# Performance work log

Hardware: AMD Instinct MI355X
Metric: run time of the kernel (lower is better)

## Reference

```python
import jax, jax.numpy as jnp
import numpy as np

BLOCK_SIZE = 2048
HEAD_SIZE = 64
N_EMBD = 768


def setup_inputs() -> dict:
    key = jax.random.key(0)
    k1, k2, k3 = jax.random.split(key, 3)
    x = jax.random.normal(k1, (8, 2048, N_EMBD), dtype=jnp.float32)
    Wq = jax.random.normal(k2, (N_EMBD, HEAD_SIZE), dtype=jnp.float32) * (N_EMBD ** -0.5)
    rel_table = jax.random.normal(k3, (2 * BLOCK_SIZE - 1, 1), dtype=jnp.float32)
    return {"x": x, "Wq": Wq, "rel_table": rel_table}


def reference(x, Wq, rel_table):
    B, T, C = x.shape
    # NOTE: original module uses self.query for q, k AND v (faithful reproduction)
    q = x @ Wq  # [B, T, H]
    k = q
    v = q
    max_rel = BLOCK_SIZE - 1
    pos = jnp.arange(T)
    rel = pos[None, :] - pos[:, None]            # [T, T]
    rel_idx = jnp.clip(rel, -max_rel, max_rel) + max_rel
    bias = rel_table[rel_idx, 0][None, :, :]     # [1, T, T]
    scores = jnp.einsum('bth,bsh->bts', q, k) * (HEAD_SIZE ** -0.5)
    scores = scores + bias
    causal = pos[None, :] <= pos[:, None]        # [T, T] lower-triangular
    scores = jnp.where(causal[None, :, :], scores, -jnp.inf)
    attn = jax.nn.softmax(scores, axis=-1)       # dropout p=0.0 -> identity
    out = jnp.einsum('bts,bsh->bth', attn, v)    # [B, T, H]
    return out
```

## Files before the change

### kernel.cpp

```cpp
#include <hip/hip_runtime.h>
#include <hip/hip_fp16.h>

typedef _Float16 half8 __attribute__((ext_vector_type(8)));
typedef _Float16 half4 __attribute__((ext_vector_type(4)));
typedef float floatx4 __attribute__((ext_vector_type(4)));

#define T_SEQ 2048
#define NB    8

#define GLOBAL_AS __attribute__((address_space(1)))
#define LDS_AS    __attribute__((address_space(3)))

__global__ __launch_bounds__(256) void prep_kernel(
    const float* __restrict__ Wq, const float* __restrict__ rel,
    _Float16* __restrict__ WqT, float* __restrict__ biasS)
{
  const int bid = blockIdx.x, tid = threadIdx.x;
  if (bid < 64) {
    for (int k = tid; k < 768; k += 256)
      WqT[bid * 768 + k] = (_Float16)Wq[k * 64 + bid];
  } else {
    for (int i = tid; i < 4095; i += 256)
      biasS[i] = rel[i] * 1.44269504f;
  }
}

__global__ __launch_bounds__(256, 2) void qproj_kernel(
    const float* __restrict__ x, const _Float16* __restrict__ WqT,
    const float* __restrict__ rel,
    _Float16* __restrict__ q16, _Float16* __restrict__ q16T,
    float* __restrict__ Ct)
{
  __shared__ __align__(16) float xbuf[16 * 772];
  __shared__ float part[2 * 16 * 66];
  __shared__ float sumsq[16];
  _Float16* qs = (_Float16*)xbuf;

  const int tid  = threadIdx.x;
  const int w    = tid >> 6, lane = tid & 63;
  const int n    = lane & 15, quad = lane >> 4;
  const int k0   = w * 192;

  const _Float16* wp = WqT + (size_t)n * 768 + k0 + quad * 8;
  half8 Breg[6][4];
  #pragma unroll
  for (int i = 0; i < 6; ++i)
    #pragma unroll
    for (int t = 0; t < 4; ++t)
      Breg[i][t] = *(const half8*)(wp + 32 * i + t * 16 * 768);

  const float b0v = rel[2047] * 1.44269504f;
  float* partw = part + (w & 1) * 1056;

  #pragma unroll 1
  for (int it = 0; it < 2; ++it) {
    const int r0 = (blockIdx.x + it * 512) * 16;

    __syncthreads();

    #pragma unroll
    for (int r = 0; r < 4; ++r) {
      #pragma unroll
      for (int c = 0; c < 3; ++c) {
        const float* gp = x + (size_t)(r0 + 4 * w + r) * 768 + c * 256 + lane * 4;
        float* lp = xbuf + (4 * w + r) * 772 + c * 256 + lane * 4;
        __builtin_amdgcn_global_load_lds((const GLOBAL_AS void*)gp,
                                         (LDS_AS void*)lp, 16, 0, 0);
      }
    }
    __builtin_amdgcn_s_waitcnt(0x0f70);
    __syncthreads();

    floatx4 acc[4];
    #pragma unroll
    for (int s = 0; s < 4; ++s) acc[s] = (floatx4){0.f, 0.f, 0.f, 0.f};

    #pragma unroll
    for (int i = 0; i < 6; ++i) {
      const float* ap = xbuf + n * 772 + k0 + 32 * i + quad * 8;
      float4 x0 = *(const float4*)ap;
      float4 x1 = *(const float4*)(ap + 4);
      half8 a;
      a[0] = (_Float16)x0.x; a[1] = (_Float16)x0.y;
      a[2] = (_Float16)x0.z; a[3] = (_Float16)x0.w;
      a[4] = (_Float16)x1.x; a[5] = (_Float16)x1.y;
      a[6] = (_Float16)x1.z; a[7] = (_Float16)x1.w;
      acc[0] = __builtin_amdgcn_mfma_f32_16x16x32_f16(a, Breg[i][0], acc[0], 0, 0, 0);
      acc[1] = __builtin_amdgcn_mfma_f32_16x16x32_f16(a, Breg[i][1], acc[1], 0, 0, 0);
      acc[2] = __builtin_amdgcn_mfma_f32_16x16x32_f16(a, Breg[i][2], acc[2], 0, 0, 0);
      acc[3] = __builtin_amdgcn_mfma_f32_16x16x32_f16(a, Breg[i][3], acc[3], 0, 0, 0);
    }

    if (w < 2) {
      #pragma unroll
      for (int sub = 0; sub < 4; ++sub)
        #pragma unroll
        for (int r = 0; r < 4; ++r)
          partw[(4 * quad + r) * 66 + sub * 16 + n] = acc[sub][r];
    }
    __syncthreads();
    if (w >= 2) {
      #pragma unroll
      for (int sub = 0; sub < 4; ++sub)
        #pragma unroll
        for (int r = 0; r < 4; ++r)
          partw[(4 * quad + r) * 66 + sub * 16 + n] += acc[sub][r];
    }
    __syncthreads();

    #pragma unroll
    for (int k = 0; k < 4; ++k) {
      int e = tid + k * 256;
      int row = e >> 6, h = e & 63;
      float s = part[row * 66 + h] + part[1056 + row * 66 + h];
      q16[(size_t)(r0 + row) * 64 + h] = (_Float16)s;
      qs[row * 66 + h] = (_Float16)s;
      float ss = s * s;
      #pragma unroll
      for (int off = 1; off < 64; off <<= 1) ss += __shfl_xor(ss, off);
      if (lane == 0) sumsq[row] = ss;
    }
    __syncthreads();

    if (tid < 16)
      Ct[r0 + tid] = sumsq[tid] * 0.18033688f + b0v + 8.0f;

    {
      const int h = tid >> 2, rq = (tid & 3) * 4;
      half4 hv;
      hv[0] = qs[(rq + 0) * 66 + h]; hv[1] = qs[(rq + 1) * 66 + h];
      hv[2] = qs[(rq + 2) * 66 + h]; hv[3] = qs[(rq + 3) * 66 + h];
      const int bb = r0 >> 11, tt = r0 & 2047;
      *(half4*)(q16T + (size_t)(bb * 64 + h) * T_SEQ + tt + rq) = hv;
    }
  }
}

__global__ __launch_bounds__(256, 2) void attn_kernel(
    const _Float16* __restrict__ q16, const _Float16* __restrict__ q16T,
    const float* __restrict__ biasS, const float* __restrict__ Ct,
    float* __restrict__ out)
{
  __shared__ __align__(16) _Float16 Pbuf[4 * 16 * 72];
  __shared__ float Obuf[4 * 16 * 65];
  __shared__ float Lbuf[4 * 16];
  __shared__ float biasL[2080];

  const int bi = blockIdx.x;
  const int b  = bi & 7;
  const int p  = bi >> 3;

  const int tid  = threadIdx.x;
  const int w    = tid >> 6;
  const int lane = tid & 63;
  const int n    = lane & 15, quad = lane >> 4;

  _Float16* Pw = Pbuf + w * 1152;
  const float ksc = 0.125f * 1.44269504f;
  const _Float16* vbase = q16T + (size_t)(b * 64 + n) * T_SEQ + quad * 8;
  const half8 ones = {(_Float16)1, (_Float16)1, (_Float16)1, (_Float16)1,
                      (_Float16)1, (_Float16)1, (_Float16)1, (_Float16)1};

  #define LOAD_KV(S0, K, V)                                                   \
    {                                                                         \
      _Pragma("unroll")                                                       \
      for (int sub = 0; sub < 4; ++sub) {                                     \
        const _Float16* kp =                                                  \
            q16 + (size_t)(b * T_SEQ + (S0) + sub * 16 + n) * 64 + quad * 8;  \
        K[2 * sub]     = *(const half8*)kp;                                   \
        K[2 * sub + 1] = *(const half8*)(kp + 32);                            \
      }                                                                       \
      _Pragma("unroll")                                                       \
      for (int sh = 0; sh < 4; ++sh) {                                        \
        V[sh]     = *(const half8*)(vbase + (size_t)(sh * 16) * T_SEQ + (S0));\
        V[4 + sh] = *(const half8*)(vbase + (size_t)(sh * 16) * T_SEQ + (S0) + 32); \
      }                                                                       \
    }

  #pragma unroll 1
  for (int ht = 0; ht < 2; ++ht) {
    const int qi = ht ? (127 - p) : p;
    const int t0 = qi * 16;
    const int kfull = t0 >> 6;

    {
      const int lo = 2032 - t0, cnt = t0 + 31;
      for (int i = tid; i < cnt; i += 256) biasL[i] = biasS[lo + i];
    }

    half8 aq0, aq1;
    {
      const _Float16* qrow = q16 + (size_t)(b * T_SEQ + t0 + n) * 64 + quad * 8;
      aq0 = *(const half8*)qrow;
      aq1 = *(const half8*)(qrow + 32);
    }
    float ctv[4];
    #pragma unroll
    for (int r = 0; r < 4; ++r)
      ctv[r] = Ct[b * T_SEQ + t0 + 4 * quad + r];

    floatx4 O[4];
    #pragma unroll
    for (int s = 0; s < 4; ++s) O[s] = (floatx4){0.f, 0.f, 0.f, 0.f};
    floatx4 den = (floatx4){0.f, 0.f, 0.f, 0.f};

    __syncthreads();

    half8 cK[8], cV[8], nK[8], nV[8];
    int kt = w;
    if (kt <= kfull) LOAD_KV(kt * 64, cK, cV);

    for (; kt <= kfull; kt += 4) {
      const int ktn = kt + 4;
      if (ktn <= kfull) LOAD_KV(ktn * 64, nK, nV);

      const int  s0 = kt * 64;
      const bool dg = (kt == kfull);
      const int  j  = (t0 - s0) >> 4;

      #pragma unroll
      for (int sub = 0; sub < 4; ++sub) {
        if (dg && sub > j) {
          #pragma unroll
          for (int r = 0; r < 4; ++r)
            Pw[(4 * quad + r) * 72 + sub * 16 + n] = (_Float16)0.f;
          continue;
        }
        floatx4 sc = (floatx4){0.f, 0.f, 0.f, 0.f};
        sc = __builtin_amdgcn_mfma_f32_16x16x32_f16(aq0, cK[2 * sub], sc, 0, 0, 0);
        sc = __builtin_amdgcn_mfma_f32_16x16x32_f16(aq1, cK[2 * sub + 1], sc, 0, 0, 0);
        const int smin = s0 + sub * 16;
        #pragma unroll
        for (int r = 0; r < 4; ++r) {
          float bv = biasL[15 + smin + n - 4 * quad - r];
          float pv = exp2f(fmaf(sc[r], ksc, bv) - ctv[r]);
          if (dg && sub == j && n > 4 * quad + r) pv = 0.f;
          Pw[(4 * quad + r) * 72 + sub * 16 + n] = (_Float16)pv;
        }
      }

      #pragma unroll
      for (int ch = 0; ch < 2; ++ch) {
        half8 pf = *(const half8*)(Pw + n * 72 + ch * 32 + quad * 8);
        den = __builtin_amdgcn_mfma_f32_16x16x32_f16(pf, ones, den, 0, 0, 0);
        #pragma unroll
        for (int sh = 0; sh < 4; ++sh)
          O[sh] = __builtin_amdgcn_mfma_f32_16x16x32_f16(pf, cV[ch * 4 + sh],
                                                         O[sh], 0, 0, 0);
      }

      #pragma unroll
      for (int i = 0; i < 8; ++i) { cK[i] = nK[i]; cV[i] = nV[i]; }
    }

    #pragma unroll
    for (int sub = 0; sub < 4; ++sub)
      #pragma unroll
      for (int r = 0; r < 4; ++r)
        Obuf[w * 1040 + (4 * quad + r) * 65 + sub * 16 + n] = O[sub][r];
    if (n == 0) {
      #pragma unroll
      for (int r = 0; r < 4; ++r)
        Lbuf[w * 16 + 4 * quad + r] = den[r];
    }
    __syncthreads();

    #pragma unroll
    for (int k = 0; k < 4; ++k) {
      const int e = tid + k * 256;
      const int row = e >> 6, h = e & 63;
      float num = Obuf[row * 65 + h]        + Obuf[1040 + row * 65 + h] +
                  Obuf[2080 + row * 65 + h] + Obuf[3120 + row * 65 + h];
      float d   = Lbuf[row] + Lbuf[16 + row] + Lbuf[32 + row] + Lbuf[48 + row];
      out[(size_t)(b * T_SEQ + t0 + row) * 64 + h] = num / d;
    }
  }
  #undef LOAD_KV
}

extern "C" void kernel_launch(void* const* d_in, const int* in_sizes, int n_in,
                              void* d_out, int out_size, void* d_ws, size_t ws_size,
                              hipStream_t stream) {
  const float* x   = (const float*)d_in[0];
  const float* Wq  = (const float*)d_in[1];
  const float* rel = (const float*)d_in[2];
  float* out = (float*)d_out;

  _Float16* q16   = (_Float16*)d_ws;
  _Float16* q16T  = q16  + (size_t)NB * T_SEQ * 64;
  _Float16* WqT   = q16T + (size_t)NB * T_SEQ * 64;
  float*    biasS = (float*)(WqT + 64 * 768);
  float*    Ct    = biasS + 4096;

  prep_kernel <<<65,  256, 0, stream>>>(Wq, rel, WqT, biasS);
  qproj_kernel<<<512, 256, 0, stream>>>(x, WqT, rel, q16, q16T, Ct);
  attn_kernel <<<512, 256, 0, stream>>>(q16, q16T, biasS, Ct, out);
}
```

Before: 134.9 us.

## Split persistent loops into one tile per block and pre-swizzle Wq fragments

The qproj and attention kernels no longer loop over two tiles per block; grids double to 1024 blocks and each block handles a single tile. Attention blocks pair light and heavy query tiles through index remapping instead of an inner loop. Wq is pre-packed in MFMA fragment order so qproj loads B fragments directly per chunk instead of holding them in registers, and x is converted to fp16 into LDS with plain loads rather than async LDS loads. The bias prescaling moves into the attention kernel, removing one prep buffer. This trades per-block setup reuse for more blocks, higher occupancy and better load balance.

```diff
diff --git a/kernel.cpp b/kernel.cpp
--- a/kernel.cpp
+++ b/kernel.cpp
@@ -8,137 +8,109 @@
 #define T_SEQ 2048
 #define NB    8
 
-#define GLOBAL_AS __attribute__((address_space(1)))
-#define LDS_AS    __attribute__((address_space(3)))
-
-__global__ __launch_bounds__(256) void prep_kernel(
-    const float* __restrict__ Wq, const float* __restrict__ rel,
-    _Float16* __restrict__ WqT, float* __restrict__ biasS)
+__global__ __launch_bounds__(64) void prep_kernel(
+    const float* __restrict__ Wq, _Float16* __restrict__ WqTs)
 {
-  const int bid = blockIdx.x, tid = threadIdx.x;
-  if (bid < 64) {
-    for (int k = tid; k < 768; k += 256)
-      WqT[bid * 768 + k] = (_Float16)Wq[k * 64 + bid];
-  } else {
-    for (int i = tid; i < 4095; i += 256)
-      biasS[i] = rel[i] * 1.44269504f;
-  }
-}
-
-__global__ __launch_bounds__(256, 2) void qproj_kernel(
-    const float* __restrict__ x, const _Float16* __restrict__ WqT,
+  const int b = blockIdx.x;
+  const int cg = b >> 2, t = b & 3;
+  const int l = threadIdx.x, n = l & 15, q = l >> 4;
+  const int h = 16 * t + n;
+  half8 v;
+  #pragma unroll
+  for (int j = 0; j < 8; ++j)
+    v[j] = (_Float16)Wq[(32 * cg + 8 * q + j) * 64 + h];
+  *(half8*)(WqTs + (size_t)b * 512 + l * 8) = v;
+}
+
+__global__ __launch_bounds__(256, 4) void qproj_kernel(
+    const float* __restrict__ x, const _Float16* __restrict__ WqTs,
     const float* __restrict__ rel,
     _Float16* __restrict__ q16, _Float16* __restrict__ q16T,
     float* __restrict__ Ct)
 {
-  __shared__ __align__(16) float xbuf[16 * 772];
-  __shared__ float part[2 * 16 * 66];
-  __shared__ float sumsq[16];
-  _Float16* qs = (_Float16*)xbuf;
+  __shared__ __align__(16) char smem[24704];
+  _Float16* xs   = (_Float16*)smem;
+  float*    cbuf = (float*)smem;
+  _Float16* qs   = (_Float16*)(smem + 16640);
+  float*    sq   = (float*)(smem + 16640 + 2112);
 
   const int tid  = threadIdx.x;
   const int w    = tid >> 6, lane = tid & 63;
   const int n    = lane & 15, quad = lane >> 4;
-  const int k0   = w * 192;
-
-  const _Float16* wp = WqT + (size_t)n * 768 + k0 + quad * 8;
-  half8 Breg[6][4];
-  #pragma unroll
-  for (int i = 0; i < 6; ++i)
-    #pragma unroll
-    for (int t = 0; t < 4; ++t)
-      Breg[i][t] = *(const half8*)(wp + 32 * i + t * 16 * 768);
+  const int r0   = blockIdx.x * 16;
+
+  #pragma unroll
+  for (int i = 0; i < 12; ++i) {
+    const int e   = tid + 256 * i;
+    const int row = e / 192, c4 = e - row * 192;
+    float4 v = *(const float4*)(x + (size_t)(r0 + row) * 768 + 4 * c4);
+    half4 hv;
+    hv[0] = (_Float16)v.x; hv[1] = (_Float16)v.y;
+    hv[2] = (_Float16)v.z; hv[3] = (_Float16)v.w;
+    *(half4*)(xs + row * 770 + 4 * c4) = hv;
+  }
+  __syncthreads();
+
+  floatx4 acc[4];
+  #pragma unroll
+  for (int s = 0; s < 4; ++s) acc[s] = (floatx4){0.f, 0.f, 0.f, 0.f};
+
+  const int k0 = w * 192;
+  #pragma unroll
+  for (int c = 0; c < 6; ++c) {
+    const int cg = w * 6 + c;
+    const _Float16* bp = WqTs + (size_t)cg * 2048 + lane * 8;
+    half8 b0 = *(const half8*)(bp);
+    half8 b1 = *(const half8*)(bp + 512);
+    half8 b2 = *(const half8*)(bp + 1024);
+    half8 b3 = *(const half8*)(bp + 1536);
+    half8 a  = *(const half8*)(xs + n * 770 + k0 + 32 * c + 8 * quad);
+    acc[0] = __builtin_amdgcn_mfma_f32_16x16x32_f16(a, b0, acc[0], 0, 0, 0);
+    acc[1] = __builtin_amdgcn_mfma_f32_16x16x32_f16(a, b1, acc[1], 0, 0, 0);
+    acc[2] = __builtin_amdgcn_mfma_f32_16x16x32_f16(a, b2, acc[2], 0, 0, 0);
+    acc[3] = __builtin_amdgcn_mfma_f32_16x16x32_f16(a, b3, acc[3], 0, 0, 0);
+  }
+  __syncthreads();
+
+  #pragma unroll
+  for (int sub = 0; sub < 4; ++sub)
+    #pragma unroll
+    for (int r = 0; r < 4; ++r)
+      cbuf[w * 1040 + (4 * quad + r) * 65 + sub * 16 + n] = acc[sub][r];
+  __syncthreads();
 
   const float b0v = rel[2047] * 1.44269504f;
-  float* partw = part + (w & 1) * 1056;
-
-  #pragma unroll 1
-  for (int it = 0; it < 2; ++it) {
-    const int r0 = (blockIdx.x + it * 512) * 16;
-
-    __syncthreads();
-
-    #pragma unroll
-    for (int r = 0; r < 4; ++r) {
-      #pragma unroll
-      for (int c = 0; c < 3; ++c) {
-        const float* gp = x + (size_t)(r0 + 4 * w + r) * 768 + c * 256 + lane * 4;
-        float* lp = xbuf + (4 * w + r) * 772 + c * 256 + lane * 4;
-        __builtin_amdgcn_global_load_lds((const GLOBAL_AS void*)gp,
-                                         (LDS_AS void*)lp, 16, 0, 0);
-      }
-    }
-    __builtin_amdgcn_s_waitcnt(0x0f70);
-    __syncthreads();
-
-    floatx4 acc[4];
-    #pragma unroll
-    for (int s = 0; s < 4; ++s) acc[s] = (floatx4){0.f, 0.f, 0.f, 0.f};
-
-    #pragma unroll
-    for (int i = 0; i < 6; ++i) {
-      const float* ap = xbuf + n * 772 + k0 + 32 * i + quad * 8;
-      float4 x0 = *(const float4*)ap;
-      float4 x1 = *(const float4*)(ap + 4);
-      half8 a;
-      a[0] = (_Float16)x0.x; a[1] = (_Float16)x0.y;
-      a[2] = (_Float16)x0.z; a[3] = (_Float16)x0.w;
-      a[4] = (_Float16)x1.x; a[5] = (_Float16)x1.y;
-      a[6] = (_Float16)x1.z; a[7] = (_Float16)x1.w;
-      acc[0] = __builtin_amdgcn_mfma_f32_16x16x32_f16(a, Breg[i][0], acc[0], 0, 0, 0);
-      acc[1] = __builtin_amdgcn_mfma_f32_16x16x32_f16(a, Breg[i][1], acc[1], 0, 0, 0);
-      acc[2] = __builtin_amdgcn_mfma_f32_16x16x32_f16(a, Breg[i][2], acc[2], 0, 0, 0);
-      acc[3] = __builtin_amdgcn_mfma_f32_16x16x32_f16(a, Breg[i][3], acc[3], 0, 0, 0);
-    }
-
-    if (w < 2) {
-      #pragma unroll
-      for (int sub = 0; sub < 4; ++sub)
-        #pragma unroll
-        for (int r = 0; r < 4; ++r)
-          partw[(4 * quad + r) * 66 + sub * 16 + n] = acc[sub][r];
-    }
-    __syncthreads();
-    if (w >= 2) {
-      #pragma unroll
-      for (int sub = 0; sub < 4; ++sub)
-        #pragma unroll
-        for (int r = 0; r < 4; ++r)
-          partw[(4 * quad + r) * 66 + sub * 16 + n] += acc[sub][r];
-    }
-    __syncthreads();
-
-    #pragma unroll
-    for (int k = 0; k < 4; ++k) {
-      int e = tid + k * 256;
-      int row = e >> 6, h = e & 63;
-      float s = part[row * 66 + h] + part[1056 + row * 66 + h];
-      q16[(size_t)(r0 + row) * 64 + h] = (_Float16)s;
-      qs[row * 66 + h] = (_Float16)s;
-      float ss = s * s;
-      #pragma unroll
-      for (int off = 1; off < 64; off <<= 1) ss += __shfl_xor(ss, off);
-      if (lane == 0) sumsq[row] = ss;
-    }
-    __syncthreads();
-
-    if (tid < 16)
-      Ct[r0 + tid] = sumsq[tid] * 0.18033688f + b0v + 8.0f;
-
-    {
-      const int h = tid >> 2, rq = (tid & 3) * 4;
-      half4 hv;
-      hv[0] = qs[(rq + 0) * 66 + h]; hv[1] = qs[(rq + 1) * 66 + h];
-      hv[2] = qs[(rq + 2) * 66 + h]; hv[3] = qs[(rq + 3) * 66 + h];
-      const int bb = r0 >> 11, tt = r0 & 2047;
-      *(half4*)(q16T + (size_t)(bb * 64 + h) * T_SEQ + tt + rq) = hv;
-    }
+  #pragma unroll
+  for (int k = 0; k < 4; ++k) {
+    const int e = tid + 256 * k;
+    const int row = e >> 6, h = e & 63;
+    float s = cbuf[row * 65 + h]        + cbuf[1040 + row * 65 + h] +
+              cbuf[2080 + row * 65 + h] + cbuf[3120 + row * 65 + h];
+    q16[(size_t)(r0 + row) * 64 + h] = (_Float16)s;
+    qs[row * 66 + h] = (_Float16)s;
+    float ss = s * s;
+    #pragma unroll
+    for (int off = 1; off < 64; off <<= 1) ss += __shfl_xor(ss, off);
+    if (lane == 0) sq[row] = ss;
+  }
+  __syncthreads();
+
+  if (tid < 16)
+    Ct[r0 + tid] = sq[tid] * 0.18033688f + b0v + 8.0f;
+
+  {
+    const int h = tid >> 2, rq = (tid & 3) * 4;
+    half4 hv;
+    hv[0] = qs[(rq + 0) * 66 + h]; hv[1] = qs[(rq + 1) * 66 + h];
+    hv[2] = qs[(rq + 2) * 66 + h]; hv[3] = qs[(rq + 3) * 66 + h];
+    const int bb = r0 >> 11, tt = r0 & 2047;
+    *(half4*)(q16T + (size_t)(bb * 64 + h) * T_SEQ + tt + rq) = hv;
   }
 }
 
 __global__ __launch_bounds__(256, 2) void attn_kernel(
     const _Float16* __restrict__ q16, const _Float16* __restrict__ q16T,
-    const float* __restrict__ biasS, const float* __restrict__ Ct,
+    const float* __restrict__ rel, const float* __restrict__ Ct,
     float* __restrict__ out)
 {
   __shared__ __align__(16) _Float16 Pbuf[4 * 16 * 72];
@@ -148,18 +120,44 @@
 
   const int bi = blockIdx.x;
   const int b  = bi & 7;
-  const int p  = bi >> 3;
+  const int u  = bi >> 3;
+  const int qi = (u < 64) ? u : 191 - u;
+  const int t0 = qi * 16;
+  const int kfull = t0 >> 6;
 
   const int tid  = threadIdx.x;
   const int w    = tid >> 6;
   const int lane = tid & 63;
   const int n    = lane & 15, quad = lane >> 4;
 
+  {
+    const int lo = 2032 - t0, cnt = t0 + 31;
+    for (int i = tid; i < cnt; i += 256) biasL[i] = rel[lo + i] * 1.44269504f;
+  }
+
+  half8 aq0, aq1;
+  {
+    const _Float16* qrow = q16 + (size_t)(b * T_SEQ + t0 + n) * 64 + quad * 8;
+    aq0 = *(const half8*)qrow;
+    aq1 = *(const half8*)(qrow + 32);
+  }
+  float ctv[4];
+  #pragma unroll
+  for (int r = 0; r < 4; ++r)
+    ctv[r] = Ct[b * T_SEQ + t0 + 4 * quad + r];
+
+  floatx4 O[4];
+  #pragma unroll
+  for (int s = 0; s < 4; ++s) O[s] = (floatx4){0.f, 0.f, 0.f, 0.f};
+  floatx4 den = (floatx4){0.f, 0.f, 0.f, 0.f};
+  const half8 ones = {(_Float16)1, (_Float16)1, (_Float16)1, (_Float16)1,
+                      (_Float16)1, (_Float16)1, (_Float16)1, (_Float16)1};
+
   _Float16* Pw = Pbuf + w * 1152;
   const float ksc = 0.125f * 1.44269504f;
   const _Float16* vbase = q16T + (size_t)(b * 64 + n) * T_SEQ + quad * 8;
-  const half8 ones = {(_Float16)1, (_Float16)1, (_Float16)1, (_Float16)1,
-                      (_Float16)1, (_Float16)1, (_Float16)1, (_Float16)1};
+
+  __syncthreads();
 
   #define LOAD_KV(S0, K, V)                                                   \
     {                                                                         \
@@ -177,105 +175,75 @@
       }                                                                       \
     }
 
-  #pragma unroll 1
-  for (int ht = 0; ht < 2; ++ht) {
-    const int qi = ht ? (127 - p) : p;
-    const int t0 = qi * 16;
-    const int kfull = t0 >> 6;
-
-    {
-      const int lo = 2032 - t0, cnt = t0 + 31;
-      for (int i = tid; i < cnt; i += 256) biasL[i] = biasS[lo + i];
+  half8 cK[8], cV[8], nK[8], nV[8];
+  int kt = w;
+  if (kt <= kfull) LOAD_KV(kt * 64, cK, cV);
+
+  for (; kt <= kfull; kt += 4) {
+    const int ktn = kt + 4;
+    if (ktn <= kfull) LOAD_KV(ktn * 64, nK, nV);
+
+    const int  s0 = kt * 64;
+    const bool dg = (kt == kfull);
+    const int  j  = (t0 - s0) >> 4;
+
+    #pragma unroll
+    for (int sub = 0; sub < 4; ++sub) {
+      if (dg && sub > j) {
+        #pragma unroll
+        for (int r = 0; r < 4; ++r)
+          Pw[(4 * quad + r) * 72 + sub * 16 + n] = (_Float16)0.f;
+        continue;
+      }
+      floatx4 sc = (floatx4){0.f, 0.f, 0.f, 0.f};
+      sc = __builtin_amdgcn_mfma_f32_16x16x32_f16(aq0, cK[2 * sub], sc, 0, 0, 0);
+      sc = __builtin_amdgcn_mfma_f32_16x16x32_f16(aq1, cK[2 * sub + 1], sc, 0, 0, 0);
+      const int smin = s0 + sub * 16;
+      #pragma unroll
+      for (int r = 0; r < 4; ++r) {
+        float bv = biasL[15 + smin + n - 4 * quad - r];
+        float pv = exp2f(fmaf(sc[r], ksc, bv) - ctv[r]);
+        if (dg && sub == j && n > 4 * quad + r) pv = 0.f;
+        Pw[(4 * quad + r) * 72 + sub * 16 + n] = (_Float16)pv;
+      }
     }
 
-    half8 aq0, aq1;
-    {
-      const _Float16* qrow = q16 + (size_t)(b * T_SEQ + t0 + n) * 64 + quad * 8;
-      aq0 = *(const half8*)qrow;
-      aq1 = *(const half8*)(qrow + 32);
+    #pragma unroll
+    for (int ch = 0; ch < 2; ++ch) {
+      half8 pf = *(const half8*)(Pw + n * 72 + ch * 32 + quad * 8);
+      den = __builtin_amdgcn_mfma_f32_16x16x32_f16(pf, ones, den, 0, 0, 0);
+      #pragma unroll
+      for (int sh = 0; sh < 4; ++sh)
+        O[sh] = __builtin_amdgcn_mfma_f32_16x16x32_f16(pf, cV[ch * 4 + sh],
+                                                       O[sh], 0, 0, 0);
     }
-    float ctv[4];
+
+    #pragma unroll
+    for (int i = 0; i < 8; ++i) { cK[i] = nK[i]; cV[i] = nV[i]; }
+  }
+  #undef LOAD_KV
+
+  #pragma unroll
+  for (int sub = 0; sub < 4; ++sub)
     #pragma unroll
     for (int r = 0; r < 4; ++r)
-      ctv[r] = Ct[b * T_SEQ + t0 + 4 * quad + r];
-
-    floatx4 O[4];
-    #pragma unroll
-    for (int s = 0; s < 4; ++s) O[s] = (floatx4){0.f, 0.f, 0.f, 0.f};
-    floatx4 den = (floatx4){0.f, 0.f, 0.f, 0.f};
-
-    __syncthreads();
-
-    half8 cK[8], cV[8], nK[8], nV[8];
-    int kt = w;
-    if (kt <= kfull) LOAD_KV(kt * 64, cK, cV);
-
-    for (; kt <= kfull; kt += 4) {
-      const int ktn = kt + 4;
-      if (ktn <= kfull) LOAD_KV(ktn * 64, nK, nV);
-
-      const int  s0 = kt * 64;
-      const bool dg = (kt == kfull);
-      const int  j  = (t0 - s0) >> 4;
-
-      #pragma unroll
-      for (int sub = 0; sub < 4; ++sub) {
-        if (dg && sub > j) {
-          #pragma unroll
-          for (int r = 0; r < 4; ++r)
-            Pw[(4 * quad + r) * 72 + sub * 16 + n] = (_Float16)0.f;
-          continue;
-        }
-        floatx4 sc = (floatx4){0.f, 0.f, 0.f, 0.f};
-        sc = __builtin_amdgcn_mfma_f32_16x16x32_f16(aq0, cK[2 * sub], sc, 0, 0, 0);
-        sc = __builtin_amdgcn_mfma_f32_16x16x32_f16(aq1, cK[2 * sub + 1], sc, 0, 0, 0);
-        const int smin = s0 + sub * 16;
-        #pragma unroll
-        for (int r = 0; r < 4; ++r) {
-          float bv = biasL[15 + smin + n - 4 * quad - r];
-          float pv = exp2f(fmaf(sc[r], ksc, bv) - ctv[r]);
-          if (dg && sub == j && n > 4 * quad + r) pv = 0.f;
-          Pw[(4 * quad + r) * 72 + sub * 16 + n] = (_Float16)pv;
-        }
-      }
-
-      #pragma unroll
-      for (int ch = 0; ch < 2; ++ch) {
-        half8 pf = *(const half8*)(Pw + n * 72 + ch * 32 + quad * 8);
-        den = __builtin_amdgcn_mfma_f32_16x16x32_f16(pf, ones, den, 0, 0, 0);
-        #pragma unroll
-        for (int sh = 0; sh < 4; ++sh)
-          O[sh] = __builtin_amdgcn_mfma_f32_16x16x32_f16(pf, cV[ch * 4 + sh],
-                                                         O[sh], 0, 0, 0);
-      }
-
-      #pragma unroll
-      for (int i = 0; i < 8; ++i) { cK[i] = nK[i]; cV[i] = nV[i]; }
-    }
-
-    #pragma unroll
-    for (int sub = 0; sub < 4; ++sub)
-      #pragma unroll
-      for (int r = 0; r < 4; ++r)
-        Obuf[w * 1040 + (4 * quad + r) * 65 + sub * 16 + n] = O[sub][r];
-    if (n == 0) {
-      #pragma unroll
-      for (int r = 0; r < 4; ++r)
-        Lbuf[w * 16 + 4 * quad + r] = den[r];
-    }
-    __syncthreads();
-
-    #pragma unroll
-    for (int k = 0; k < 4; ++k) {
-      const int e = tid + k * 256;
-      const int row = e >> 6, h = e & 63;
-      float num = Obuf[row * 65 + h]        + Obuf[1040 + row * 65 + h] +
-                  Obuf[2080 + row * 65 + h] + Obuf[3120 + row * 65 + h];
-      float d   = Lbuf[row] + Lbuf[16 + row] + Lbuf[32 + row] + Lbuf[48 + row];
-      out[(size_t)(b * T_SEQ + t0 + row) * 64 + h] = num / d;
-    }
-  }
-  #undef LOAD_KV
+      Obuf[w * 1040 + (4 * quad + r) * 65 + sub * 16 + n] = O[sub][r];
+  if (n == 0) {
+    #pragma unroll
+    for (int r = 0; r < 4; ++r)
+      Lbuf[w * 16 + 4 * quad + r] = den[r];
+  }
+  __syncthreads();
+
+  #pragma unroll
+  for (int k = 0; k < 4; ++k) {
+    const int e = tid + k * 256;
+    const int row = e >> 6, h = e & 63;
+    float num = Obuf[row * 65 + h]        + Obuf[1040 + row * 65 + h] +
+                Obuf[2080 + row * 65 + h] + Obuf[3120 + row * 65 + h];
+    float d   = Lbuf[row] + Lbuf[16 + row] + Lbuf[32 + row] + Lbuf[48 + row];
+    out[(size_t)(b * T_SEQ + t0 + row) * 64 + h] = num / d;
+  }
 }
 
 extern "C" void kernel_launch(void* const* d_in, const int* in_sizes, int n_in,
@@ -288,11 +256,10 @@
 
   _Float16* q16   = (_Float16*)d_ws;
   _Float16* q16T  = q16  + (size_t)NB * T_SEQ * 64;
-  _Float16* WqT   = q16T + (size_t)NB * T_SEQ * 64;
-  float*    biasS = (float*)(WqT + 64 * 768);
-  float*    Ct    = biasS + 4096;
-
-  prep_kernel <<<65,  256, 0, stream>>>(Wq, rel, WqT, biasS);
-  qproj_kernel<<<512, 256, 0, stream>>>(x, WqT, rel, q16, q16T, Ct);
-  attn_kernel <<<512, 256, 0, stream>>>(q16, q16T, biasS, Ct, out);
-}
+  _Float16* WqTs  = q16T + (size_t)NB * T_SEQ * 64;
+  float*    Ct    = (float*)(WqTs + 96 * 512);
+
+  prep_kernel <<<96,    64, 0, stream>>>(Wq, WqTs);
+  qproj_kernel<<<1024, 256, 0, stream>>>(x, WqTs, rel, q16, q16T, Ct);
+  attn_kernel <<<1024, 256, 0, stream>>>(q16, q16T, rel, Ct, out);
+}
```

New measurement: 129.1 us. 1.04x faster.
